# Performance work log

Measured on AMD Instinct MI355X. Metric: run time of the kernel, lower is better.

## Reference

```python
import jax, jax.numpy as jnp
import numpy as np

B, L, D_MODEL, H = 4, 2048, 1024, 16
HD = D_MODEL // H  # head_dim = 64


def _rope_tables(seq_len, dim, dtype):
    inv_freq = 1.0 / (10000.0 ** (jnp.arange(0, dim, 2, dtype=jnp.float32) / dim))
    t = jnp.arange(seq_len, dtype=jnp.float32)
    freqs = jnp.outer(t, inv_freq)  # (S, dim/2)
    return jnp.cos(freqs).astype(dtype), jnp.sin(freqs).astype(dtype)


def _apply_rope(x):
    # x: (B, H, S, d)
    cos, sin = _rope_tables(x.shape[-2], x.shape[-1], x.dtype)  # (S, d/2)
    x_even = x[..., 0::2]
    x_odd = x[..., 1::2]
    out_even = x_even * cos - x_odd * sin
    out_odd = x_even * sin + x_odd * cos
    return jnp.stack([out_even, out_odd], axis=-1).reshape(x.shape)


def setup_inputs() -> dict:
    key = jax.random.key(0)
    ks = jax.random.split(key, 9)
    s = 1.0 / np.sqrt(D_MODEL)
    inp = {
        "query": jax.random.normal(ks[0], (B, L, D_MODEL), dtype=jnp.float32),
        "Wq": jax.random.uniform(ks[1], (D_MODEL, D_MODEL), jnp.float32, -s, s),
        "bq": jax.random.uniform(ks[2], (D_MODEL,), jnp.float32, -s, s),
        "Wk": jax.random.uniform(ks[3], (D_MODEL, D_MODEL), jnp.float32, -s, s),
        "bk": jax.random.uniform(ks[4], (D_MODEL,), jnp.float32, -s, s),
        "Wv": jax.random.uniform(ks[5], (D_MODEL, D_MODEL), jnp.float32, -s, s),
        "bv": jax.random.uniform(ks[6], (D_MODEL,), jnp.float32, -s, s),
        "Wo": jax.random.uniform(ks[7], (D_MODEL, D_MODEL), jnp.float32, -s, s),
        "bo": jax.random.uniform(ks[8], (D_MODEL,), jnp.float32, -s, s),
    }
    return inp


def reference(query, Wq, bq, Wk, bk, Wv, bv, Wo, bo):
    Bq, Lq, _ = query.shape
    # projections (torch Linear: x @ W.T + b), split into heads -> (B, H, L, d)
    def proj(x, W, b):
        y = x @ W.T + b
        return y.reshape(Bq, Lq, H, HD).transpose(0, 2, 1, 3)
    q = _apply_rope(proj(query, Wq, bq))
    k = _apply_rope(proj(query, Wk, bk))
    v = proj(query, Wv, bv)
    scores = jnp.einsum("bhqd,bhkd->bhqk", q, k) / np.sqrt(HD)
    causal_mask = jnp.triu(jnp.ones((Lq, Lq), dtype=bool), k=1)
    scores = jnp.where(causal_mask[None, None, :, :], -jnp.inf, scores)
    attn = jax.nn.softmax(scores, axis=-1)
    out = jnp.einsum("bhqk,bhkd->bhqd", attn, v)
    out = out.transpose(0, 2, 1, 3).reshape(Bq, Lq, D_MODEL)
    return out @ Wo.T + bo
```

## Files before the change

### kernel.cpp

```cpp
#include <hip/hip_runtime.h>
#include <hip/hip_bf16.h>
#include <math.h>

#define L_SEQ  2048
#define DMODEL 1024
#define NHEAD  16
#define HEADD  64

typedef __attribute__((ext_vector_type(8))) short short8;
typedef __attribute__((ext_vector_type(4))) short short4v;
typedef __attribute__((ext_vector_type(4))) float f32x4;

#define LDA 32

static __device__ __forceinline__ unsigned short f2bf(float f) {
    unsigned int u = __float_as_uint(f);
    unsigned int r = (u + 0x7fffu + ((u >> 16) & 1u)) >> 16;
    return (unsigned short)r;
}

static __device__ __forceinline__ void dma16(const unsigned short* g, unsigned short* l) {
    __builtin_amdgcn_global_load_lds((const __attribute__((address_space(1))) void*)g,
                                     (__attribute__((address_space(3))) void*)l, 16, 0, 0);
}

__global__ void cvt_f32_bf16(const float* __restrict__ in,
                             unsigned short* __restrict__ out, int n4) {
    int i = blockIdx.x * blockDim.x + threadIdx.x;
    if (i >= n4) return;
    float4 v = reinterpret_cast<const float4*>(in)[i];
    ushort4 o;
    o.x = f2bf(v.x); o.y = f2bf(v.y); o.z = f2bf(v.z); o.w = f2bf(v.w);
    reinterpret_cast<ushort4*>(out)[i] = o;
}

__global__ void cvt_weights(const float* __restrict__ Wq, const float* __restrict__ Wk,
                            const float* __restrict__ Wv, const float* __restrict__ Wo,
                            unsigned short* __restrict__ dst) {
    int i = blockIdx.x * blockDim.x + threadIdx.x;
    int which = i >> 18;
    const float* src = which == 0 ? Wq : which == 1 ? Wk : which == 2 ? Wv : Wo;
    float4 v = reinterpret_cast<const float4*>(src)[i & 262143];
    ushort4 o;
    o.x = f2bf(v.x); o.y = f2bf(v.y); o.z = f2bf(v.z); o.w = f2bf(v.w);
    reinterpret_cast<ushort4*>(dst)[i] = o;
}

__global__ void build_rope(float* __restrict__ tab) {
    int i = blockIdx.x * blockDim.x + threadIdx.x;
    int lpos = i >> 5, i2 = i & 31;
    float inv_f = expf(-0.28782313662425574f * (float)i2);
    float ang = (float)lpos * inv_f;
    tab[2 * i]     = cosf(ang);
    tab[2 * i + 1] = sinf(ang);
}

#define BKP 32

__global__ __launch_bounds__(256) void proj_qkv(
    const unsigned short* __restrict__ X,
    const unsigned short* __restrict__ Wqkv,
    const float* __restrict__ bq_,
    const float* __restrict__ bk_,
    const float* __restrict__ bv_,
    const float* __restrict__ rope,
    unsigned short* __restrict__ Qb,
    unsigned short* __restrict__ Kb,
    unsigned short* __restrict__ Vr)
{
    __shared__ unsigned short a_lds[3][128 * BKP];
    __shared__ unsigned short b_lds[3][128 * BKP];

    const int tid  = threadIdx.x;
    const int lane = tid & 63;
    const int w    = tid >> 6;
    const int wm   = w & 1, wn = w >> 1;
    const int quad = lane >> 4, l16 = lane & 15;

    const int orig = blockIdx.y * 24 + blockIdx.x;
    const int swz  = (orig & 7) * 192 + (orig >> 3);
    const int bx   = swz % 24;
    const int by   = swz / 24;
    const int m0   = by * 128;
    const int n0   = bx * 128;

    const int sel = bx >> 3;
    const float* bias   = sel == 0 ? bq_ : (sel == 1 ? bk_ : bv_);
    unsigned short* out = sel == 0 ? Qb  : (sel == 1 ? Kb  : Vr);

    const int st_row = lane >> 2;
    const int st_col = (((lane & 3) ^ ((lane >> 3) & 3)) << 3);
    const int rd = ((quad ^ ((l16 >> 1) & 3)) << 3);

    f32x4 acc[4][4];
#pragma unroll
    for (int i = 0; i < 4; ++i)
#pragma unroll
        for (int j = 0; j < 4; ++j) acc[i][j] = (f32x4){0.f, 0.f, 0.f, 0.f};

    const unsigned short* Xs = X    + (size_t)(m0 + w * 32 + st_row) * DMODEL + st_col;
    const unsigned short* Ws = Wqkv + (size_t)(n0 + w * 32 + st_row) * DMODEL + st_col;
    const int ldsA0 = (w * 32) * BKP, ldsA1 = (w * 32 + 16) * BKP;

#pragma unroll
    for (int p = 0; p < 2; ++p) {
        const int kk = p * BKP;
        dma16(Xs + kk,               &a_lds[p][ldsA0]);
        dma16(Xs + 16 * DMODEL + kk, &a_lds[p][ldsA1]);
        dma16(Ws + kk,               &b_lds[p][ldsA0]);
        dma16(Ws + 16 * DMODEL + kk, &b_lds[p][ldsA1]);
    }
    asm volatile("s_waitcnt vmcnt(4)" ::: "memory");
    __builtin_amdgcn_s_barrier();

    for (int kt = 0; kt < 32; ++kt) {
        const int slot = kt % 3;
        const int ps   = (kt + 2) % 3;
        const int kk   = ((kt + 2) & 31) * BKP;

        short8 af[4], bf[2];
#pragma unroll
        for (int i = 0; i < 4; ++i)
            af[i] = *reinterpret_cast<const short8*>(
                &a_lds[slot][(wm * 64 + i * 16 + l16) * BKP + rd]);
#pragma unroll
        for (int j = 0; j < 2; ++j)
            bf[j] = *reinterpret_cast<const short8*>(
                &b_lds[slot][(wn * 64 + j * 16 + l16) * BKP + rd]);
        dma16(Xs + kk,               &a_lds[ps][ldsA0]);
        dma16(Xs + 16 * DMODEL + kk, &a_lds[ps][ldsA1]);
        __builtin_amdgcn_s_barrier();
        asm volatile("s_waitcnt lgkmcnt(0)" ::: "memory");
        __builtin_amdgcn_sched_barrier(0);
        __builtin_amdgcn_s_setprio(1);
#pragma unroll
        for (int i = 0; i < 4; ++i)
#pragma unroll
            for (int j = 0; j < 2; ++j)
                acc[i][j] = __builtin_amdgcn_mfma_f32_16x16x32_bf16(af[i], bf[j], acc[i][j], 0, 0, 0);
        __builtin_amdgcn_s_setprio(0);
        __builtin_amdgcn_s_barrier();

#pragma unroll
        for (int j = 0; j < 2; ++j)
            bf[j] = *reinterpret_cast<const short8*>(
                &b_lds[slot][(wn * 64 + (2 + j) * 16 + l16) * BKP + rd]);
        dma16(Ws + kk,               &b_lds[ps][ldsA0]);
        dma16(Ws + 16 * DMODEL + kk, &b_lds[ps][ldsA1]);
        __builtin_amdgcn_s_barrier();
        asm volatile("s_waitcnt lgkmcnt(0)" ::: "memory");
        __builtin_amdgcn_sched_barrier(0);
        __builtin_amdgcn_s_setprio(1);
#pragma unroll
        for (int i = 0; i < 4; ++i)
#pragma unroll
            for (int j = 0; j < 2; ++j)
                acc[i][2 + j] = __builtin_amdgcn_mfma_f32_16x16x32_bf16(af[i], bf[j], acc[i][2 + j], 0, 0, 0);
        __builtin_amdgcn_s_setprio(0);
        asm volatile("s_waitcnt vmcnt(4)" ::: "memory");
        __builtin_amdgcn_s_barrier();
    }
    asm volatile("s_waitcnt vmcnt(0)" ::: "memory");

#pragma unroll
    for (int jf = 0; jf < 4; ++jf) {
        int nn = (bx & 7) * 128 + wn * 64 + jf * 16 + l16;
        float bval = bias[nn];
        int d  = nn & (HEADD - 1);
        int h  = nn >> 6;
        float sgn = (d & 1) ? 1.0f : -1.0f;
        int i2 = d >> 1;
#pragma unroll
        for (int mf = 0; mf < 4; ++mf) {
#pragma unroll
            for (int r = 0; r < 4; ++r) {
                int m_g = m0 + wm * 64 + mf * 16 + quad * 4 + r;
                float v = acc[mf][jf][r] + bval;
                int b    = m_g >> 11;
                int lpos = m_g & (L_SEQ - 1);
                if (sel < 2) {
                    float p = __shfl_xor(v, 1);
                    float2 cs = *reinterpret_cast<const float2*>(&rope[(size_t)(lpos * 32 + i2) * 2]);
                    v = v * cs.x + sgn * cs.y * p;
                    if (sel == 0) v *= 0.18033688011112042f;
                }
                out[((size_t)(b * NHEAD + h) * L_SEQ + lpos) * HEADD + d] = f2bf(v);
            }
        }
    }
}

__global__ __launch_bounds__(256) void transpose_v(
    const unsigned short* __restrict__ Vr, unsigned short* __restrict__ Vt)
{
    __shared__ unsigned short tile[64 * 72];
    const int tid = threadIdx.x;
    const int bh  = blockIdx.y;
    const int l0  = blockIdx.x * 64;
#pragma unroll
    for (int t = 0; t < 2; ++t) {
        int c = tid + t * 256;
        int row = c >> 3, cc = (c & 7) << 3;
        int4 v = *reinterpret_cast<const int4*>(Vr + ((size_t)bh * L_SEQ + l0 + row) * HEADD + cc);
        *reinterpret_cast<int4*>(&tile[row * 72 + cc]) = v;
    }
    __syncthreads();
#pragma unroll
    for (int t = 0; t < 2; ++t) {
        int c = tid + t * 256;
        int d = c >> 3, lc = (c & 7) << 3;
        union { unsigned short u[8]; int4 v; } tt;
#pragma unroll
        for (int j = 0; j < 8; ++j) tt.u[j] = tile[(lc + j) * 72 + d];
        *reinterpret_cast<int4*>(Vt + ((size_t)bh * HEADD + d) * L_SEQ + l0 + lc) = tt.v;
    }
}

#define LDK 88

__global__ __launch_bounds__(256) void attn_fwd(
    const unsigned short* __restrict__ Q,
    const unsigned short* __restrict__ K,
    const unsigned short* __restrict__ Vt,
    unsigned short* __restrict__ Oa)
{
    __shared__ unsigned short k_lds[64 * LDK];
    __shared__ unsigned short v_lds[64 * LDK];
    const int tid  = threadIdx.x;
    const int lane = tid & 63;
    const int w    = tid >> 6;
    const int quad = lane >> 4, l16 = lane & 15;
    const int pair = blockIdx.x;
    const int bh   = blockIdx.y;
    const size_t base = (size_t)bh * L_SEQ * HEADD;

    const int srow0 = tid >> 3;
    const int scc   = (tid & 7) << 3;
    const int b = bh >> 4, h = bh & 15;

    for (int half = 0; half < 2; ++half) {
        const int qb = half ? (31 - pair) : pair;
        const int qrow = qb * 64 + w * 16 + l16;

        short8 qf[2];
#pragma unroll
        for (int ks = 0; ks < 2; ++ks)
            qf[ks] = *reinterpret_cast<const short8*>(Q + base + (size_t)qrow * HEADD + ks * 32 + quad * 8);

        f32x4 o[4];
#pragma unroll
        for (int nt = 0; nt < 4; ++nt) o[nt] = (f32x4){0.f, 0.f, 0.f, 0.f};
        float lsum = 0.f;

        int4 ka0 = *reinterpret_cast<const int4*>(K  + base + (size_t)srow0 * HEADD + scc);
        int4 ka1 = *reinterpret_cast<const int4*>(K  + base + (size_t)(srow0 + 32) * HEADD + scc);
        int4 va0 = *reinterpret_cast<const int4*>(Vt + base + (size_t)srow0 * L_SEQ + scc);
        int4 va1 = *reinterpret_cast<const int4*>(Vt + base + (size_t)(srow0 + 32) * L_SEQ + scc);

        for (int kb = 0; kb <= qb; ++kb) {
            __syncthreads();
            *reinterpret_cast<int4*>(&k_lds[srow0 * LDK + scc])        = ka0;
            *reinterpret_cast<int4*>(&k_lds[(srow0 + 32) * LDK + scc]) = ka1;
            *reinterpret_cast<int4*>(&v_lds[srow0 * LDK + scc])        = va0;
            *reinterpret_cast<int4*>(&v_lds[(srow0 + 32) * LDK + scc]) = va1;
            __syncthreads();

            if (kb < qb) {
                int kn = kb + 1;
                ka0 = *reinterpret_cast<const int4*>(K  + base + (size_t)(kn * 64 + srow0) * HEADD + scc);
                ka1 = *reinterpret_cast<const int4*>(K  + base + (size_t)(kn * 64 + srow0 + 32) * HEADD + scc);
                va0 = *reinterpret_cast<const int4*>(Vt + base + (size_t)srow0 * L_SEQ + kn * 64 + scc);
                va1 = *reinterpret_cast<const int4*>(Vt + base + (size_t)(srow0 + 32) * L_SEQ + kn * 64 + scc);
            }

            f32x4 st[4];
#pragma unroll
            for (int nt = 0; nt < 4; ++nt) st[nt] = (f32x4){0.f, 0.f, 0.f, 0.f};
#pragma unroll
            for (int ks = 0; ks < 2; ++ks)
#pragma unroll
                for (int nt = 0; nt < 4; ++nt) {
                    short8 kf = *reinterpret_cast<const short8*>(&k_lds[(nt * 16 + l16) * LDK + ks * 32 + quad * 8]);
                    st[nt] = __builtin_amdgcn_mfma_f32_16x16x32_bf16(kf, qf[ks], st[nt], 0, 0, 0);
                }

            if (kb == qb) {
#pragma unroll
                for (int nt = 0; nt < 4; ++nt)
#pragma unroll
                    for (int r = 0; r < 4; ++r) {
                        int seqcol = kb * 64 + nt * 16 + quad * 4 + r;
                        if (seqcol > qrow) st[nt][r] = -INFINITY;
                    }
            }

            short4v pfrag[4];
#pragma unroll
            for (int nt = 0; nt < 4; ++nt) {
                float p0 = __builtin_amdgcn_exp2f(st[nt][0]);
                float p1 = __builtin_amdgcn_exp2f(st[nt][1]);
                float p2 = __builtin_amdgcn_exp2f(st[nt][2]);
                float p3 = __builtin_amdgcn_exp2f(st[nt][3]);
                lsum += (p0 + p1) + (p2 + p3);
                unsigned u0 = __float_as_uint(p0) + 0x8000u;
                unsigned u1 = __float_as_uint(p1) + 0x8000u;
                unsigned u2 = __float_as_uint(p2) + 0x8000u;
                unsigned u3 = __float_as_uint(p3) + 0x8000u;
                union { unsigned u[2]; short4v v; } pk;
                pk.u[0] = (u0 >> 16) | (u1 & 0xffff0000u);
                pk.u[1] = (u2 >> 16) | (u3 & 0xffff0000u);
                pfrag[nt] = pk.v;
            }

#pragma unroll
            for (int c = 0; c < 4; ++c)
#pragma unroll
                for (int nt2 = 0; nt2 < 4; ++nt2) {
                    short4v vf = *reinterpret_cast<const short4v*>(
                        &v_lds[(nt2 * 16 + l16) * LDK + c * 16 + quad * 4]);
                    o[nt2] = __builtin_amdgcn_mfma_f32_16x16x16bf16_1k(pfrag[c], vf, o[nt2], 0, 0, 0);
                }
        }

        lsum += __shfl_xor(lsum, 16);
        lsum += __shfl_xor(lsum, 32);
        float rs[4];
#pragma unroll
        for (int r = 0; r < 4; ++r) rs[r] = __shfl(lsum, quad * 4 + r);
#pragma unroll
        for (int r = 0; r < 4; ++r) {
            float inv = 1.0f / rs[r];
            int lg = qb * 64 + w * 16 + quad * 4 + r;
#pragma unroll
            for (int nt = 0; nt < 4; ++nt) {
                int d = nt * 16 + l16;
                Oa[(size_t)(b * L_SEQ + lg) * DMODEL + h * HEADD + d] = f2bf(o[nt][r] * inv);
            }
        }
    }
}

__global__ __launch_bounds__(256) void out_gemm(
    const unsigned short* __restrict__ X,
    const unsigned short* __restrict__ W,
    const float* __restrict__ bias,
    float* __restrict__ out)
{
    __shared__ unsigned short a_lds[2][128 * LDA];
    __shared__ unsigned short b_lds[2][128 * LDA];
    const int tid  = threadIdx.x;
    const int lane = tid & 63;
    const int w    = tid >> 6;
    const int wm   = w & 1, wn = w >> 1;
    const int quad = lane >> 4, l16 = lane & 15;
    const int m0 = blockIdx.y * 128;
    const int n0 = blockIdx.x * 128;

    f32x4 acc[4][4];
#pragma unroll
    for (int i = 0; i < 4; ++i)
#pragma unroll
        for (int j = 0; j < 4; ++j) acc[i][j] = (f32x4){0.f, 0.f, 0.f, 0.f};

    const int drow = lane >> 2;
    const int dcol = (lane & 3) << 3;

#pragma unroll
    for (int t = 0; t < 2; ++t) {
        int r0 = w * 32 + t * 16;
        dma16(X + (size_t)(m0 + r0 + drow) * DMODEL + dcol, &a_lds[0][r0 * LDA]);
        dma16(W + (size_t)(n0 + r0 + drow) * DMODEL + dcol, &b_lds[0][r0 * LDA]);
    }

    for (int it = 0; it < 32; ++it) {
        __syncthreads();
        int cb = it & 1;
        if (it < 31) {
            int kk = (it + 1) * 32;
#pragma unroll
            for (int t = 0; t < 2; ++t) {
                int r0 = w * 32 + t * 16;
                dma16(X + (size_t)(m0 + r0 + drow) * DMODEL + kk + dcol, &a_lds[cb ^ 1][r0 * LDA]);
                dma16(W + (size_t)(n0 + r0 + drow) * DMODEL + kk + dcol, &b_lds[cb ^ 1][r0 * LDA]);
            }
        }
        short8 af[4], bf[4];
#pragma unroll
        for (int mt = 0; mt < 4; ++mt)
            af[mt] = *reinterpret_cast<const short8*>(&a_lds[cb][(wm * 64 + mt * 16 + l16) * LDA + quad * 8]);
#pragma unroll
        for (int nt = 0; nt < 4; ++nt)
            bf[nt] = *reinterpret_cast<const short8*>(&b_lds[cb][(wn * 64 + nt * 16 + l16) * LDA + quad * 8]);
#pragma unroll
        for (int mt = 0; mt < 4; ++mt)
#pragma unroll
            for (int nt = 0; nt < 4; ++nt)
                acc[mt][nt] = __builtin_amdgcn_mfma_f32_16x16x32_bf16(af[mt], bf[nt], acc[mt][nt], 0, 0, 0);
    }

#pragma unroll
    for (int nt = 0; nt < 4; ++nt) {
        int n_g = n0 + wn * 64 + nt * 16 + l16;
        float bv = bias[n_g];
#pragma unroll
        for (int mt = 0; mt < 4; ++mt)
#pragma unroll
            for (int r = 0; r < 4; ++r) {
                int m_g = m0 + wm * 64 + mt * 16 + quad * 4 + r;
                out[(size_t)m_g * DMODEL + n_g] = acc[mt][nt][r] + bv;
            }
    }
}

extern "C" void kernel_launch(void* const* d_in, const int* in_sizes, int n_in,
                              void* d_out, int out_size, void* d_ws, size_t ws_size,
                              hipStream_t stream) {
    const float* query = (const float*)d_in[0];
    const float* Wq = (const float*)d_in[1];
    const float* bq = (const float*)d_in[2];
    const float* Wk = (const float*)d_in[3];
    const float* bk = (const float*)d_in[4];
    const float* Wv = (const float*)d_in[5];
    const float* bv = (const float*)d_in[6];
    const float* Wo = (const float*)d_in[7];
    const float* bo = (const float*)d_in[8];
    float* out = (float*)d_out;

    unsigned short* ws  = (unsigned short*)d_ws;
    unsigned short* xb  = ws;
    unsigned short* wqb = xb  + (size_t)8388608;
    unsigned short* wkb = wqb + 1048576;
    unsigned short* wvb = wkb + 1048576;
    unsigned short* wob = wvb + 1048576;
    unsigned short* Qb  = wob + 1048576;
    unsigned short* Kb  = Qb  + 8388608;
    unsigned short* Vr  = Kb  + 8388608;
    unsigned short* Vtb = Vr  + 8388608;
    unsigned short* Ab  = Vtb + 8388608;
    float* rope = (float*)(Ab + 8388608);

    (void)wkb; (void)wvb;

    build_rope<<<256, 256, 0, stream>>>(rope);
    cvt_f32_bf16<<<8192, 256, 0, stream>>>(query, xb, 2097152);
    cvt_weights<<<4096, 256, 0, stream>>>(Wq, Wk, Wv, Wo, wqb);

    proj_qkv<<<dim3(24, 64), 256, 0, stream>>>(xb, wqb, bq, bk, bv, rope, Qb, Kb, Vr);
    transpose_v<<<dim3(32, 64), 256, 0, stream>>>(Vr, Vtb);
    attn_fwd<<<dim3(16, 64), 256, 0, stream>>>(Qb, Kb, Vtb, Ab);
    out_gemm<<<dim3(8, 64), 256, 0, stream>>>(Ab, wob, bo, out);
}
```

Measured before the change: 326.0 us.

## Simplify QKV GEMM pipeline and port triple-buffered swizzled pipeline to out_gemm

```diff
diff --git a/kernel.cpp b/kernel.cpp
--- a/kernel.cpp
+++ b/kernel.cpp
@@ -118,44 +118,28 @@
         const int ps   = (kt + 2) % 3;
         const int kk   = ((kt + 2) & 31) * BKP;
 
-        short8 af[4], bf[2];
+        dma16(Xs + kk,               &a_lds[ps][ldsA0]);
+        dma16(Xs + 16 * DMODEL + kk, &a_lds[ps][ldsA1]);
+        dma16(Ws + kk,               &b_lds[ps][ldsA0]);
+        dma16(Ws + 16 * DMODEL + kk, &b_lds[ps][ldsA1]);
+
+        short8 af[4], bf[4];
 #pragma unroll
         for (int i = 0; i < 4; ++i)
             af[i] = *reinterpret_cast<const short8*>(
                 &a_lds[slot][(wm * 64 + i * 16 + l16) * BKP + rd]);
 #pragma unroll
-        for (int j = 0; j < 2; ++j)
+        for (int j = 0; j < 4; ++j)
             bf[j] = *reinterpret_cast<const short8*>(
                 &b_lds[slot][(wn * 64 + j * 16 + l16) * BKP + rd]);
-        dma16(Xs + kk,               &a_lds[ps][ldsA0]);
-        dma16(Xs + 16 * DMODEL + kk, &a_lds[ps][ldsA1]);
-        __builtin_amdgcn_s_barrier();
         asm volatile("s_waitcnt lgkmcnt(0)" ::: "memory");
         __builtin_amdgcn_sched_barrier(0);
         __builtin_amdgcn_s_setprio(1);
 #pragma unroll
         for (int i = 0; i < 4; ++i)
 #pragma unroll
-            for (int j = 0; j < 2; ++j)
+            for (int j = 0; j < 4; ++j)
                 acc[i][j] = __builtin_amdgcn_mfma_f32_16x16x32_bf16(af[i], bf[j], acc[i][j], 0, 0, 0);
-        __builtin_amdgcn_s_setprio(0);
-        __builtin_amdgcn_s_barrier();
-
-#pragma unroll
-        for (int j = 0; j < 2; ++j)
-            bf[j] = *reinterpret_cast<const short8*>(
-                &b_lds[slot][(wn * 64 + (2 + j) * 16 + l16) * BKP + rd]);
-        dma16(Ws + kk,               &b_lds[ps][ldsA0]);
-        dma16(Ws + 16 * DMODEL + kk, &b_lds[ps][ldsA1]);
-        __builtin_amdgcn_s_barrier();
-        asm volatile("s_waitcnt lgkmcnt(0)" ::: "memory");
-        __builtin_amdgcn_sched_barrier(0);
-        __builtin_amdgcn_s_setprio(1);
-#pragma unroll
-        for (int i = 0; i < 4; ++i)
-#pragma unroll
-            for (int j = 0; j < 2; ++j)
-                acc[i][2 + j] = __builtin_amdgcn_mfma_f32_16x16x32_bf16(af[i], bf[j], acc[i][2 + j], 0, 0, 0);
         __builtin_amdgcn_s_setprio(0);
         asm volatile("s_waitcnt vmcnt(4)" ::: "memory");
         __builtin_amdgcn_s_barrier();
@@ -346,15 +330,22 @@
     const float* __restrict__ bias,
     float* __restrict__ out)
 {
-    __shared__ unsigned short a_lds[2][128 * LDA];
-    __shared__ unsigned short b_lds[2][128 * LDA];
+    __shared__ unsigned short a_lds[3][128 * BKP];
+    __shared__ unsigned short b_lds[3][128 * BKP];
     const int tid  = threadIdx.x;
     const int lane = tid & 63;
     const int w    = tid >> 6;
     const int wm   = w & 1, wn = w >> 1;
     const int quad = lane >> 4, l16 = lane & 15;
-    const int m0 = blockIdx.y * 128;
-    const int n0 = blockIdx.x * 128;
+
+    const int orig = blockIdx.y * 8 + blockIdx.x;
+    const int swz  = (orig & 7) * 64 + (orig >> 3);
+    const int m0 = (swz >> 3) * 128;
+    const int n0 = (swz & 7) * 128;
+
+    const int st_row = lane >> 2;
+    const int st_col = (((lane & 3) ^ ((lane >> 3) & 3)) << 3);
+    const int rd = ((quad ^ ((l16 >> 1) & 3)) << 3);
 
     f32x4 acc[4][4];
 #pragma unroll
@@ -362,41 +353,53 @@
 #pragma unroll
         for (int j = 0; j < 4; ++j) acc[i][j] = (f32x4){0.f, 0.f, 0.f, 0.f};
 
-    const int drow = lane >> 2;
-    const int dcol = (lane & 3) << 3;
-
-#pragma unroll
-    for (int t = 0; t < 2; ++t) {
-        int r0 = w * 32 + t * 16;
-        dma16(X + (size_t)(m0 + r0 + drow) * DMODEL + dcol, &a_lds[0][r0 * LDA]);
-        dma16(W + (size_t)(n0 + r0 + drow) * DMODEL + dcol, &b_lds[0][r0 * LDA]);
-    }
-
-    for (int it = 0; it < 32; ++it) {
-        __syncthreads();
-        int cb = it & 1;
-        if (it < 31) {
-            int kk = (it + 1) * 32;
-#pragma unroll
-            for (int t = 0; t < 2; ++t) {
-                int r0 = w * 32 + t * 16;
-                dma16(X + (size_t)(m0 + r0 + drow) * DMODEL + kk + dcol, &a_lds[cb ^ 1][r0 * LDA]);
-                dma16(W + (size_t)(n0 + r0 + drow) * DMODEL + kk + dcol, &b_lds[cb ^ 1][r0 * LDA]);
-            }
-        }
+    const unsigned short* Xs = X + (size_t)(m0 + w * 32 + st_row) * DMODEL + st_col;
+    const unsigned short* Ws = W + (size_t)(n0 + w * 32 + st_row) * DMODEL + st_col;
+    const int ldsA0 = (w * 32) * BKP, ldsA1 = (w * 32 + 16) * BKP;
+
+#pragma unroll
+    for (int p = 0; p < 2; ++p) {
+        const int kk = p * BKP;
+        dma16(Xs + kk,               &a_lds[p][ldsA0]);
+        dma16(Xs + 16 * DMODEL + kk, &a_lds[p][ldsA1]);
+        dma16(Ws + kk,               &b_lds[p][ldsA0]);
+        dma16(Ws + 16 * DMODEL + kk, &b_lds[p][ldsA1]);
+    }
+    asm volatile("s_waitcnt vmcnt(4)" ::: "memory");
+    __builtin_amdgcn_s_barrier();
+
+    for (int kt = 0; kt < 32; ++kt) {
+        const int slot = kt % 3;
+        const int ps   = (kt + 2) % 3;
+        const int kk   = ((kt + 2) & 31) * BKP;
+
+        dma16(Xs + kk,               &a_lds[ps][ldsA0]);
+        dma16(Xs + 16 * DMODEL + kk, &a_lds[ps][ldsA1]);
+        dma16(Ws + kk,               &b_lds[ps][ldsA0]);
+        dma16(Ws + 16 * DMODEL + kk, &b_lds[ps][ldsA1]);
+
         short8 af[4], bf[4];
 #pragma unroll
-        for (int mt = 0; mt < 4; ++mt)
-            af[mt] = *reinterpret_cast<const short8*>(&a_lds[cb][(wm * 64 + mt * 16 + l16) * LDA + quad * 8]);
-#pragma unroll
-        for (int nt = 0; nt < 4; ++nt)
-            bf[nt] = *reinterpret_cast<const short8*>(&b_lds[cb][(wn * 64 + nt * 16 + l16) * LDA + quad * 8]);
-#pragma unroll
-        for (int mt = 0; mt < 4; ++mt)
-#pragma unroll
-            for (int nt = 0; nt < 4; ++nt)
-                acc[mt][nt] = __builtin_amdgcn_mfma_f32_16x16x32_bf16(af[mt], bf[nt], acc[mt][nt], 0, 0, 0);
-    }
+        for (int i = 0; i < 4; ++i)
+            af[i] = *reinterpret_cast<const short8*>(
+                &a_lds[slot][(wm * 64 + i * 16 + l16) * BKP + rd]);
+#pragma unroll
+        for (int j = 0; j < 4; ++j)
+            bf[j] = *reinterpret_cast<const short8*>(
+                &b_lds[slot][(wn * 64 + j * 16 + l16) * BKP + rd]);
+        asm volatile("s_waitcnt lgkmcnt(0)" ::: "memory");
+        __builtin_amdgcn_sched_barrier(0);
+        __builtin_amdgcn_s_setprio(1);
+#pragma unroll
+        for (int i = 0; i < 4; ++i)
+#pragma unroll
+            for (int j = 0; j < 4; ++j)
+                acc[i][j] = __builtin_amdgcn_mfma_f32_16x16x32_bf16(af[i], bf[j], acc[i][j], 0, 0, 0);
+        __builtin_amdgcn_s_setprio(0);
+        asm volatile("s_waitcnt vmcnt(4)" ::: "memory");
+        __builtin_amdgcn_s_barrier();
+    }
+    asm volatile("s_waitcnt vmcnt(0)" ::: "memory");
 
 #pragma unroll
     for (int nt = 0; nt < 4; ++nt) {
```

Measured after the change: 361.1 us. 1.11x slower.
